# Kernel optimization log

Measured on AMD Instinct MI355X. Metric: run time of the kernel, lower is better.

## Reference

```python
import jax, jax.numpy as jnp
import numpy as np


def setup_inputs() -> dict:
    key = jax.random.key(0)
    ks = jax.random.split(key, 6)
    B, T, E = 4, 1024, 1024
    H, D = 16, 64  # num_heads = embed_size // head_size
    s = 0.02
    x = jax.random.normal(ks[0], (B, T, E), dtype=jnp.float32)
    Wq = jax.random.normal(ks[1], (H, D, E), dtype=jnp.float32) * s
    Wk = jax.random.normal(ks[2], (H, D, E), dtype=jnp.float32) * s
    Wv = jax.random.normal(ks[3], (H, D, E), dtype=jnp.float32) * s
    Wp = jax.random.normal(ks[4], (E, E), dtype=jnp.float32) * s
    bp = jnp.zeros((E,), dtype=jnp.float32)
    return {"x": x, "Wq": Wq, "Wk": Wk, "Wv": Wv, "Wp": Wp, "bp": bp}


def reference(x, Wq, Wk, Wv, Wp, bp):
    # x: [B, T, E]; Wq/Wk/Wv: [H, D, E] (per-head Linear(E, D, bias=False) weights)
    B, T, E = x.shape
    H, D, _ = Wq.shape
    scale = 1.0 / jnp.sqrt(jnp.asarray(D, dtype=x.dtype))
    # per-head projections, vectorized over heads (same math as the ModuleList loop)
    q = jnp.einsum('bte,hde->bhtd', x, Wq)
    k = jnp.einsum('bte,hde->bhtd', x, Wk)
    v = jnp.einsum('bte,hde->bhtd', x, Wv)
    scores = jnp.einsum('bhtd,bhsd->bhts', q, k) * scale  # [B,H,T,T]
    causal = jnp.tril(jnp.ones((T, T), dtype=bool))
    scores = jnp.where(causal[None, None], scores, jnp.finfo(x.dtype).min)
    att = jax.nn.softmax(scores, axis=-1)  # attention dropout: identity in eval
    o = jnp.einsum('bhts,bhsd->bhtd', att, v)
    # concat heads along channel dim (head order = module list order)
    o = o.transpose(0, 2, 1, 3).reshape(B, T, H * D)
    # output projection (nn.Linear: y = o @ Wp.T + bp); dropout: identity in eval
    return o @ Wp.T + bp
```

## Files before the change

kernel.cpp:

```cpp
#include <hip/hip_runtime.h>


#define T_SZ 1024
#define E_SZ 1024
#define H_SZ 16
#define D_SZ 64

typedef __attribute__((ext_vector_type(8))) short bf16x8;
typedef __attribute__((ext_vector_type(4))) short bf16x4;
typedef __attribute__((ext_vector_type(4))) float f32x4;

static __device__ __forceinline__ unsigned short f2b(float f) {
  unsigned int u = __builtin_bit_cast(unsigned int, f);
  u += 0x7fffu + ((u >> 16) & 1u);
  return (unsigned short)(u >> 16);
}

static __device__ __forceinline__ unsigned int cvt_pk(float lo, float hi) {
  unsigned int r;
  asm("v_cvt_pk_bf16_f32 %0, %1, %2" : "=v"(r) : "v"(lo), "v"(hi));
  return r;
}

static __device__ __forceinline__ void load_lds16(const void* g, void* l) {
  __builtin_amdgcn_global_load_lds(
      (const __attribute__((address_space(1))) void*)g,
      (__attribute__((address_space(3))) void*)l, 16, 0, 0);
}

__global__ void cast_all(const float* __restrict__ x, const float* __restrict__ wq,
                         const float* __restrict__ wk, const float* __restrict__ wv,
                         const float* __restrict__ wp,
                         unsigned short* __restrict__ xb,
                         unsigned short* __restrict__ wqkvb,
                         unsigned short* __restrict__ wpb) {
  int b = blockIdx.x;
  const float4* src;
  ushort4* dst;
  int i;
  if (b < 4096) {
    src = (const float4*)x; dst = (ushort4*)xb; i = b * 256 + threadIdx.x;
  } else {
    int a = (b - 4096) >> 10;
    i = ((b - 4096) & 1023) * 256 + threadIdx.x;
    src = (const float4*)(a == 0 ? wq : a == 1 ? wk : a == 2 ? wv : wp);
    dst = (ushort4*)(a == 3 ? wpb : wqkvb + (size_t)a * 1048576);
  }
  float4 v = src[i];
  ushort4 o;
  o.x = f2b(v.x); o.y = f2b(v.y); o.z = f2b(v.z); o.w = f2b(v.w);
  dst[i] = o;
}

template <int EPI>
__global__ void gemm_bt(const unsigned short* __restrict__ A,
                        const unsigned short* __restrict__ Bm,
                        int M, int N, int K,
                        float* __restrict__ outF, const float* __restrict__ bias,
                        unsigned short* __restrict__ Qb,
                        unsigned short* __restrict__ Kb,
                        unsigned short* __restrict__ Vtb) {
  __shared__ __align__(16) char lds[65536];
  const int tid = threadIdx.x;
  const int wid = tid >> 6;
  const int lane = tid & 63;
  const int llo = lane & 15, lhi = lane >> 4;
  const int row0 = blockIdx.x * 128, col0 = blockIdx.y * 128;
  const int wr = (wid >> 1) * 64, wc = (wid & 1) * 64;
  const int swl = ((llo >> 2) & 3) << 5;

  f32x4 acc[4][4];
#pragma unroll
  for (int m = 0; m < 4; ++m)
#pragma unroll
    for (int n = 0; n < 4; ++n) {
      f32x4 z = {0.f, 0.f, 0.f, 0.f};
      acc[m][n] = z;
    }

  auto stage = [&](int kt, char* base) {
#pragma unroll
    for (int c = 0; c < 4; ++c) {
      int off = c * 4096 + tid * 16;
      int r = off >> 7, cb = off & 127;
      int sb = cb ^ (((r >> 2) & 3) << 5);
      load_lds16((const char*)A + ((size_t)(row0 + r) * K + kt) * 2 + sb,
                 base + c * 4096 + wid * 1024);
      load_lds16((const char*)Bm + ((size_t)(col0 + r) * K + kt) * 2 + sb,
                 base + 16384 + c * 4096 + wid * 1024);
    }
  };

  stage(0, lds);
  __syncthreads();
  int buf = 0;

  for (int kt = 0; kt < K; kt += 64) {
    char* cur = lds + buf * 32768;
    if (kt + 64 < K) stage(kt + 64, lds + (buf ^ 1) * 32768);

    bf16x8 af[4][2], bfr[4][2];
#pragma unroll
    for (int m = 0; m < 4; ++m)
#pragma unroll
      for (int kk = 0; kk < 2; ++kk)
        af[m][kk] = *reinterpret_cast<const bf16x8*>(
            cur + (wr + m * 16 + llo) * 128 + ((kk * 64 + lhi * 16) ^ swl));
#pragma unroll
    for (int n = 0; n < 4; ++n)
#pragma unroll
      for (int kk = 0; kk < 2; ++kk)
        bfr[n][kk] = *reinterpret_cast<const bf16x8*>(
            cur + 16384 + (wc + n * 16 + llo) * 128 + ((kk * 64 + lhi * 16) ^ swl));
#pragma unroll
    for (int m = 0; m < 4; ++m)
#pragma unroll
      for (int n = 0; n < 4; ++n)
#pragma unroll
        for (int kk = 0; kk < 2; ++kk)
          acc[m][n] = __builtin_amdgcn_mfma_f32_16x16x32_bf16(af[m][kk], bfr[n][kk],
                                                              acc[m][n], 0, 0, 0);
    __syncthreads();
    buf ^= 1;
  }

#pragma unroll
  for (int m = 0; m < 4; ++m)
#pragma unroll
    for (int n = 0; n < 4; ++n) {
      const int grow0 = row0 + wr + m * 16 + lhi * 4;
      const int gcol = col0 + wc + n * 16 + llo;
      if (EPI == 0) {
        int b = grow0 >> 10, t0 = grow0 & 1023;
        int which = gcol >> 10, hd = gcol & 1023;
        int h = hd >> 6, d = hd & 63;
        if (which == 2) {
          unsigned int w0 = cvt_pk(acc[m][n][0], acc[m][n][1]);
          unsigned int w1 = cvt_pk(acc[m][n][2], acc[m][n][3]);
          unsigned long long pk = ((unsigned long long)w1 << 32) | w0;
          *reinterpret_cast<unsigned long long*>(
              Vtb + (((size_t)(b * H_SZ + h)) * D_SZ + d) * T_SZ + t0) = pk;
        } else {
          unsigned short* dst = which ? Kb : Qb;
#pragma unroll
          for (int r = 0; r < 4; ++r)
            dst[(((size_t)(b * H_SZ + h)) * T_SZ + t0 + r) * D_SZ + d] =
                f2b(acc[m][n][r]);
        }
      } else {
#pragma unroll
        for (int r = 0; r < 4; ++r)
          outF[(size_t)(grow0 + r) * N + gcol] = acc[m][n][r] + bias[gcol];
      }
    }
}

__global__ void attn_kernel(const unsigned short* __restrict__ Q,
                            const unsigned short* __restrict__ K,
                            const unsigned short* __restrict__ Vt,
                            unsigned short* __restrict__ O) {
  __shared__ __align__(16) char smem[32768];
  const int tid = threadIdx.x, wid = tid >> 6, lane = tid & 63;
  const int llo = lane & 15, lhi = lane >> 4;
  const int fid = blockIdx.y * 8 + blockIdx.x;
  const int wi = (fid & 7) * 64 + (fid >> 3);
  const int blkx = wi & 7;
  const int bh = wi >> 3;
  const size_t bhbase = (size_t)bh * (T_SZ * D_SZ);
  char* Ks = smem;
  char* Vs = smem + 8192;
  char* Ps = smem + 16384 + wid * 2048;

  const int qrow = blkx * 128 + wid * 16 + llo;
  const int myqt = 2 * blkx + (wid >> 2);
  const int last = 2 * blkx + 1;
  bf16x8 bq[2];
  {
    const unsigned short* qp = Q + bhbase + (size_t)qrow * D_SZ + lhi * 8;
    bq[0] = *reinterpret_cast<const bf16x8*>(qp);
    bq[1] = *reinterpret_cast<const bf16x8*>(qp + 32);
  }

  const int soff = tid * 16;
  const int srow = soff >> 7;
  const int sinb = soff & 127;
  const int slds = srow * 128 + (sinb ^ ((srow & 7) << 4));

  bf16x8 kreg, vreg;
  kreg = *reinterpret_cast<const bf16x8*>(K + bhbase + (size_t)srow * D_SZ + (sinb >> 1));
  vreg = *reinterpret_cast<const bf16x8*>(Vt + bhbase + (size_t)srow * T_SZ + (sinb >> 1));

  f32x4 oacc[4];
#pragma unroll
  for (int dc = 0; dc < 4; ++dc) {
    f32x4 z = {0.f, 0.f, 0.f, 0.f};
    oacc[dc] = z;
  }
  float mrun = -1e30f, lrun = 0.f;
  const float scale = 0.125f;

  for (int it = 0; it <= last; ++it) {
    __syncthreads();
    *reinterpret_cast<bf16x8*>(Ks + slds) = kreg;
    *reinterpret_cast<bf16x8*>(Vs + slds) = vreg;
    if (it < last) {
      const int kv = (it + 1) * 64;
      kreg = *reinterpret_cast<const bf16x8*>(
          K + bhbase + (size_t)(kv + srow) * D_SZ + (sinb >> 1));
      vreg = *reinterpret_cast<const bf16x8*>(
          Vt + bhbase + (size_t)srow * T_SZ + kv + (sinb >> 1));
    }
    __syncthreads();

    const int kv = it * 64;
    if (it <= myqt) {
      f32x4 sacc[4];
#pragma unroll
      for (int c = 0; c < 4; ++c) { f32x4 z = {0.f, 0.f, 0.f, 0.f}; sacc[c] = z; }
      __builtin_amdgcn_s_setprio(1);
#pragma unroll
      for (int seg = 0; seg < 2; ++seg)
#pragma unroll
        for (int c = 0; c < 4; ++c) {
          int key = c * 16 + llo;
          bf16x8 ak = *reinterpret_cast<const bf16x8*>(
              Ks + key * 128 + ((seg * 64 + lhi * 16) ^ ((key & 7) << 4)));
          sacc[c] = __builtin_amdgcn_mfma_f32_16x16x32_bf16(ak, bq[seg], sacc[c], 0, 0, 0);
        }
      __builtin_amdgcn_s_setprio(0);

      const bool diag = (it == myqt);
      float p[4][4];
      float pm = -1e30f;
#pragma unroll
      for (int c = 0; c < 4; ++c)
#pragma unroll
        for (int r = 0; r < 4; ++r) {
          float s = sacc[c][r] * scale;
          if (diag && (kv + c * 16 + lhi * 4 + r > qrow)) s = -1e30f;
          p[c][r] = s;
          pm = fmaxf(pm, s);
        }
      pm = fmaxf(pm, __shfl_xor(pm, 16, 64));
      pm = fmaxf(pm, __shfl_xor(pm, 32, 64));
      if (!__all(pm - mrun <= 8.0f)) {
        float mnew = fmaxf(mrun, pm);
        float alpha = __expf(mrun - mnew);
        mrun = mnew;
        lrun *= alpha;
#pragma unroll
        for (int dc = 0; dc < 4; ++dc)
#pragma unroll
          for (int r = 0; r < 4; ++r) oacc[dc][r] *= alpha;
      }

      float ps = 0.f;
#pragma unroll
      for (int c = 0; c < 4; ++c) {
#pragma unroll
        for (int r = 0; r < 4; ++r) {
          p[c][r] = __expf(p[c][r] - mrun);
          ps += p[c][r];
        }
        unsigned int w0 = cvt_pk(p[c][0], p[c][1]);
        unsigned int w1 = cvt_pk(p[c][2], p[c][3]);
        unsigned long long packed = ((unsigned long long)w1 << 32) | w0;
        *reinterpret_cast<bf16x4*>(
            Ps + llo * 128 + ((c * 32 + lhi * 8) ^ ((llo & 7) << 4))) =
            __builtin_bit_cast(bf16x4, packed);
      }
      asm volatile("s_waitcnt lgkmcnt(0)" ::: "memory");
      __builtin_amdgcn_sched_barrier(0);

      ps += __shfl_xor(ps, 16, 64);
      ps += __shfl_xor(ps, 32, 64);
      lrun += ps;

      __builtin_amdgcn_s_setprio(1);
#pragma unroll
      for (int seg = 0; seg < 2; ++seg) {
        bf16x8 bp = *reinterpret_cast<const bf16x8*>(
            Ps + llo * 128 + ((seg * 64 + lhi * 16) ^ ((llo & 7) << 4)));
#pragma unroll
        for (int dc = 0; dc < 4; ++dc) {
          int d = dc * 16 + llo;
          bf16x8 av = *reinterpret_cast<const bf16x8*>(
              Vs + d * 128 + ((seg * 64 + lhi * 16) ^ ((d & 7) << 4)));
          oacc[dc] = __builtin_amdgcn_mfma_f32_16x16x32_bf16(av, bp, oacc[dc], 0, 0, 0);
        }
      }
      __builtin_amdgcn_s_setprio(0);
    }
  }

  const int b = bh >> 4, h = bh & 15;
  float inv = 1.f / lrun;
#pragma unroll
  for (int dc = 0; dc < 4; ++dc) {
    unsigned int w0 = cvt_pk(oacc[dc][0] * inv, oacc[dc][1] * inv);
    unsigned int w1 = cvt_pk(oacc[dc][2] * inv, oacc[dc][3] * inv);
    unsigned int* op = reinterpret_cast<unsigned int*>(
        O + ((size_t)b * T_SZ + qrow) * E_SZ + h * D_SZ + dc * 16 + lhi * 4);
    op[0] = w0;
    op[1] = w1;
  }
}

extern "C" void kernel_launch(void* const* d_in, const int* in_sizes, int n_in,
                              void* d_out, int out_size, void* d_ws, size_t ws_size,
                              hipStream_t stream) {
  const float* x  = (const float*)d_in[0];
  const float* Wq = (const float*)d_in[1];
  const float* Wk = (const float*)d_in[2];
  const float* Wv = (const float*)d_in[3];
  const float* Wp = (const float*)d_in[4];
  const float* bp = (const float*)d_in[5];
  float* out = (float*)d_out;

  char* ws = (char*)d_ws;
  unsigned short* xb   = (unsigned short*)(ws);
  unsigned short* wqkv = (unsigned short*)(ws + (8u << 20));
  unsigned short* wp   = (unsigned short*)(ws + (14u << 20));
  unsigned short* Qb   = (unsigned short*)(ws + (16u << 20));
  unsigned short* Kb   = (unsigned short*)(ws + (24u << 20));
  unsigned short* Vtb  = (unsigned short*)(ws + (32u << 20));
  unsigned short* Ob   = (unsigned short*)(ws + (40u << 20));

  cast_all<<<8192, 256, 0, stream>>>(x, Wq, Wk, Wv, Wp, xb, wqkv, wp);

  gemm_bt<0><<<dim3(32, 24), 256, 0, stream>>>(xb, wqkv, 4096, 3072, 1024,
                                               nullptr, nullptr, Qb, Kb, Vtb);
  attn_kernel<<<dim3(8, 64), 512, 0, stream>>>(Qb, Kb, Vtb, Ob);
  gemm_bt<1><<<dim3(32, 8), 256, 0, stream>>>(Ob, wp, 4096, 1024, 1024,
                                              out, bp, nullptr, nullptr, nullptr);
}
```

Baseline: 91.39 us.

## Load K and V directly from global memory instead of shared staging

The attention kernel no longer stages K and V tiles through LDS with block-wide barriers. Each wave now reads its K and V MFMA operands straight from global memory (relying on L2/L1 caching) and iterates only up to its own causal tile count. This removes both __syncthreads per iteration and halves LDS use. In exchange each wave issues redundant global loads for the same tiles and exposes global memory latency directly to the MFMA chain, with no prefetch.

```diff
diff --git a/kernel.cpp b/kernel.cpp
--- a/kernel.cpp
+++ b/kernel.cpp
@@ -159,7 +159,7 @@
                             const unsigned short* __restrict__ K,
                             const unsigned short* __restrict__ Vt,
                             unsigned short* __restrict__ O) {
-  __shared__ __align__(16) char smem[32768];
+  __shared__ __align__(16) char smem[16384];
   const int tid = threadIdx.x, wid = tid >> 6, lane = tid & 63;
   const int llo = lane & 15, lhi = lane >> 4;
   const int fid = blockIdx.y * 8 + blockIdx.x;
@@ -167,28 +167,18 @@
   const int blkx = wi & 7;
   const int bh = wi >> 3;
   const size_t bhbase = (size_t)bh * (T_SZ * D_SZ);
-  char* Ks = smem;
-  char* Vs = smem + 8192;
-  char* Ps = smem + 16384 + wid * 2048;
+  char* Ps = smem + wid * 2048;
 
   const int qrow = blkx * 128 + wid * 16 + llo;
   const int myqt = 2 * blkx + (wid >> 2);
-  const int last = 2 * blkx + 1;
   bf16x8 bq[2];
   {
     const unsigned short* qp = Q + bhbase + (size_t)qrow * D_SZ + lhi * 8;
     bq[0] = *reinterpret_cast<const bf16x8*>(qp);
     bq[1] = *reinterpret_cast<const bf16x8*>(qp + 32);
   }
-
-  const int soff = tid * 16;
-  const int srow = soff >> 7;
-  const int sinb = soff & 127;
-  const int slds = srow * 128 + (sinb ^ ((srow & 7) << 4));
-
-  bf16x8 kreg, vreg;
-  kreg = *reinterpret_cast<const bf16x8*>(K + bhbase + (size_t)srow * D_SZ + (sinb >> 1));
-  vreg = *reinterpret_cast<const bf16x8*>(Vt + bhbase + (size_t)srow * T_SZ + (sinb >> 1));
+  const unsigned short* Kp = K + bhbase;
+  const unsigned short* Vp = Vt + bhbase;
 
   f32x4 oacc[4];
 #pragma unroll
@@ -199,98 +189,83 @@
   float mrun = -1e30f, lrun = 0.f;
   const float scale = 0.125f;
 
-  for (int it = 0; it <= last; ++it) {
-    __syncthreads();
-    *reinterpret_cast<bf16x8*>(Ks + slds) = kreg;
-    *reinterpret_cast<bf16x8*>(Vs + slds) = vreg;
-    if (it < last) {
-      const int kv = (it + 1) * 64;
-      kreg = *reinterpret_cast<const bf16x8*>(
-          K + bhbase + (size_t)(kv + srow) * D_SZ + (sinb >> 1));
-      vreg = *reinterpret_cast<const bf16x8*>(
-          Vt + bhbase + (size_t)srow * T_SZ + kv + (sinb >> 1));
-    }
-    __syncthreads();
-
+  for (int it = 0; it <= myqt; ++it) {
     const int kv = it * 64;
-    if (it <= myqt) {
-      f32x4 sacc[4];
-#pragma unroll
-      for (int c = 0; c < 4; ++c) { f32x4 z = {0.f, 0.f, 0.f, 0.f}; sacc[c] = z; }
-      __builtin_amdgcn_s_setprio(1);
-#pragma unroll
-      for (int seg = 0; seg < 2; ++seg)
-#pragma unroll
-        for (int c = 0; c < 4; ++c) {
-          int key = c * 16 + llo;
-          bf16x8 ak = *reinterpret_cast<const bf16x8*>(
-              Ks + key * 128 + ((seg * 64 + lhi * 16) ^ ((key & 7) << 4)));
-          sacc[c] = __builtin_amdgcn_mfma_f32_16x16x32_bf16(ak, bq[seg], sacc[c], 0, 0, 0);
-        }
-      __builtin_amdgcn_s_setprio(0);
-
-      const bool diag = (it == myqt);
-      float p[4][4];
-      float pm = -1e30f;
-#pragma unroll
-      for (int c = 0; c < 4; ++c)
-#pragma unroll
-        for (int r = 0; r < 4; ++r) {
-          float s = sacc[c][r] * scale;
-          if (diag && (kv + c * 16 + lhi * 4 + r > qrow)) s = -1e30f;
-          p[c][r] = s;
-          pm = fmaxf(pm, s);
-        }
-      pm = fmaxf(pm, __shfl_xor(pm, 16, 64));
-      pm = fmaxf(pm, __shfl_xor(pm, 32, 64));
-      if (!__all(pm - mrun <= 8.0f)) {
-        float mnew = fmaxf(mrun, pm);
-        float alpha = __expf(mrun - mnew);
-        mrun = mnew;
-        lrun *= alpha;
-#pragma unroll
-        for (int dc = 0; dc < 4; ++dc)
-#pragma unroll
-          for (int r = 0; r < 4; ++r) oacc[dc][r] *= alpha;
-      }
-
-      float ps = 0.f;
+
+    f32x4 sacc[4];
+#pragma unroll
+    for (int c = 0; c < 4; ++c) { f32x4 z = {0.f, 0.f, 0.f, 0.f}; sacc[c] = z; }
+    __builtin_amdgcn_s_setprio(1);
+#pragma unroll
+    for (int seg = 0; seg < 2; ++seg)
 #pragma unroll
       for (int c = 0; c < 4; ++c) {
-#pragma unroll
-        for (int r = 0; r < 4; ++r) {
-          p[c][r] = __expf(p[c][r] - mrun);
-          ps += p[c][r];
-        }
-        unsigned int w0 = cvt_pk(p[c][0], p[c][1]);
-        unsigned int w1 = cvt_pk(p[c][2], p[c][3]);
-        unsigned long long packed = ((unsigned long long)w1 << 32) | w0;
-        *reinterpret_cast<bf16x4*>(
-            Ps + llo * 128 + ((c * 32 + lhi * 8) ^ ((llo & 7) << 4))) =
-            __builtin_bit_cast(bf16x4, packed);
-      }
-      asm volatile("s_waitcnt lgkmcnt(0)" ::: "memory");
-      __builtin_amdgcn_sched_barrier(0);
-
-      ps += __shfl_xor(ps, 16, 64);
-      ps += __shfl_xor(ps, 32, 64);
-      lrun += ps;
-
-      __builtin_amdgcn_s_setprio(1);
-#pragma unroll
-      for (int seg = 0; seg < 2; ++seg) {
-        bf16x8 bp = *reinterpret_cast<const bf16x8*>(
-            Ps + llo * 128 + ((seg * 64 + lhi * 16) ^ ((llo & 7) << 4)));
-#pragma unroll
-        for (int dc = 0; dc < 4; ++dc) {
-          int d = dc * 16 + llo;
-          bf16x8 av = *reinterpret_cast<const bf16x8*>(
-              Vs + d * 128 + ((seg * 64 + lhi * 16) ^ ((d & 7) << 4)));
-          oacc[dc] = __builtin_amdgcn_mfma_f32_16x16x32_bf16(av, bp, oacc[dc], 0, 0, 0);
-        }
-      }
-      __builtin_amdgcn_s_setprio(0);
-    }
+        bf16x8 ak = *reinterpret_cast<const bf16x8*>(
+            Kp + (size_t)(kv + c * 16 + llo) * D_SZ + seg * 32 + lhi * 8);
+        sacc[c] = __builtin_amdgcn_mfma_f32_16x16x32_bf16(ak, bq[seg], sacc[c], 0, 0, 0);
+      }
+    __builtin_amdgcn_s_setprio(0);
+
+    const bool diag = (it == myqt);
+    float p[4][4];
+    float pm = -1e30f;
+#pragma unroll
+    for (int c = 0; c < 4; ++c)
+#pragma unroll
+      for (int r = 0; r < 4; ++r) {
+        float s = sacc[c][r] * scale;
+        if (diag && (kv + c * 16 + lhi * 4 + r > qrow)) s = -1e30f;
+        p[c][r] = s;
+        pm = fmaxf(pm, s);
+      }
+    pm = fmaxf(pm, __shfl_xor(pm, 16, 64));
+    pm = fmaxf(pm, __shfl_xor(pm, 32, 64));
+    if (!__all(pm - mrun <= 8.0f)) {
+      float mnew = fmaxf(mrun, pm);
+      float alpha = __expf(mrun - mnew);
+      mrun = mnew;
+      lrun *= alpha;
+#pragma unroll
+      for (int dc = 0; dc < 4; ++dc)
+#pragma unroll
+        for (int r = 0; r < 4; ++r) oacc[dc][r] *= alpha;
+    }
+
+    float ps = 0.f;
+#pragma unroll
+    for (int c = 0; c < 4; ++c) {
+#pragma unroll
+      for (int r = 0; r < 4; ++r) {
+        p[c][r] = __expf(p[c][r] - mrun);
+        ps += p[c][r];
+      }
+      unsigned int w0 = cvt_pk(p[c][0], p[c][1]);
+      unsigned int w1 = cvt_pk(p[c][2], p[c][3]);
+      unsigned long long packed = ((unsigned long long)w1 << 32) | w0;
+      *reinterpret_cast<bf16x4*>(
+          Ps + llo * 128 + ((c * 32 + lhi * 8) ^ ((llo & 7) << 4))) =
+          __builtin_bit_cast(bf16x4, packed);
+    }
+    asm volatile("s_waitcnt lgkmcnt(0)" ::: "memory");
+    __builtin_amdgcn_sched_barrier(0);
+
+    ps += __shfl_xor(ps, 16, 64);
+    ps += __shfl_xor(ps, 32, 64);
+    lrun += ps;
+
+    __builtin_amdgcn_s_setprio(1);
+#pragma unroll
+    for (int seg = 0; seg < 2; ++seg) {
+      bf16x8 bp = *reinterpret_cast<const bf16x8*>(
+          Ps + llo * 128 + ((seg * 64 + lhi * 16) ^ ((llo & 7) << 4)));
+#pragma unroll
+      for (int dc = 0; dc < 4; ++dc) {
+        bf16x8 av = *reinterpret_cast<const bf16x8*>(
+            Vp + (size_t)(dc * 16 + llo) * T_SZ + kv + seg * 32 + lhi * 8);
+        oacc[dc] = __builtin_amdgcn_mfma_f32_16x16x32_bf16(av, bp, oacc[dc], 0, 0, 0);
+      }
+    }
+    __builtin_amdgcn_s_setprio(0);
   }
 
   const int b = bh >> 4, h = bh & 15;
```

After: 170.6 us. +86.7%, slower.
